# Kernel tuning notes

Hardware: AMD Instinct MI355X
Metric: run time of the kernel (lower is better)

## Reference

```python
import jax, jax.numpy as jnp
import numpy as np

N_EXPERTS = 8
D_MODEL = 1024
D_FF = 2048
NUM_TOKENS = 16384


def setup_inputs() -> dict:
    key = jax.random.key(0)
    k1, k2, k3, k4 = jax.random.split(key, 4)
    x = jax.random.normal(k1, (NUM_TOKENS, D_MODEL), dtype=jnp.float32)
    expert_indices = jax.random.randint(k2, (NUM_TOKENS,), 0, N_EXPERTS, dtype=jnp.int32)
    # init per nn.init.normal_(std=0.02)
    gate_up_weight = 0.02 * jax.random.normal(k3, (N_EXPERTS, 2 * D_FF, D_MODEL), dtype=jnp.float32)
    down_weight = 0.02 * jax.random.normal(k4, (N_EXPERTS, D_MODEL, D_FF), dtype=jnp.float32)
    return {"x": x, "expert_indices": expert_indices,
            "gate_up_weight": gate_up_weight, "down_weight": down_weight}


def reference(x, expert_indices, gate_up_weight, down_weight):
    # Faithful math: each token t uses expert e = expert_indices[t]:
    #   combined = x @ gate_up_weight[e].T ; gate, up = split ; h = silu(gate)*up
    #   out = h @ down_weight[e].T
    # Implemented as a fixed loop over the (small) expert set with masked
    # accumulation, avoiding the original's per-token [2F,D] weight gather.
    n_experts = gate_up_weight.shape[0]
    d_ff = down_weight.shape[2]
    out = jnp.zeros((x.shape[0], down_weight.shape[1]), dtype=x.dtype)
    for e in range(n_experts):
        combined = x @ gate_up_weight[e].T                  # [T, 2*d_ff]
        gate, up = combined[:, :d_ff], combined[:, d_ff:]
        hidden = jax.nn.silu(gate) * up                     # [T, d_ff]
        o = hidden @ down_weight[e].T                       # [T, d_model]
        out = out + jnp.where((expert_indices == e)[:, None], o, 0.0)
    return out
```

## Files before the change

### kernel.cpp

```cpp
#include <hip/hip_runtime.h>

#define NTOK 16384
#define DM 1024
#define DFF 2048
#define NE 8

typedef unsigned short u16;
typedef __attribute__((ext_vector_type(8))) short bf16x8;
typedef __attribute__((ext_vector_type(4))) float f32x4;

__device__ __forceinline__ u16 f2bf(float f) {
  unsigned u = __float_as_uint(f);
  u += 0x7fff + ((u >> 16) & 1);
  return (u16)(u >> 16);
}

__device__ __forceinline__ void async16(const void* g, void* l) {
  __builtin_amdgcn_global_load_lds(
      (const __attribute__((address_space(1))) unsigned int*)g,
      (__attribute__((address_space(3))) unsigned int*)l, 16, 0, 0);
}

__global__ void k_count(const int* __restrict__ idx, int* __restrict__ counts) {
  int t = blockIdx.x * 256 + threadIdx.x;
  atomicAdd(&counts[idx[t]], 1);
}

__global__ void k_offsets(int* __restrict__ c) {
  if (threadIdx.x == 0) {
    int acc = 0;
    for (int e = 0; e < NE; e++) { c[8 + e] = acc; c[16 + e] = acc; acc += c[e]; }
  }
}

__global__ void k_scatter(const int* __restrict__ idx, int* __restrict__ cursor,
                          int* __restrict__ tl) {
  int t = blockIdx.x * 256 + threadIdx.x;
  int pos = atomicAdd(&cursor[idx[t]], 1);
  tl[pos] = t;
}

__global__ void k_cvt(const float* __restrict__ s, u16* __restrict__ d) {
  size_t i = ((size_t)blockIdx.x * 256 + threadIdx.x) * 4;
  float4 v = *(const float4*)(s + i);
  ushort4 o;
  o.x = f2bf(v.x); o.y = f2bf(v.y); o.z = f2bf(v.z); o.w = f2bf(v.w);
  *(ushort4*)(d + i) = o;
}

__global__ __launch_bounds__(512, 2) void k_gemm1(
    const u16* __restrict__ xb, const u16* __restrict__ wgu,
    u16* __restrict__ hid, const int* __restrict__ tl,
    const int* __restrict__ offs, const int* __restrict__ counts) {
  int wg = blockIdx.x;
  int e = wg & 7;
  int r = wg >> 3;
  int by = r / 9;
  int bx = r - by * 9;
  int Me = counts[e];
  int m0 = bx * 256;
  if (m0 >= Me) return;
  int n0 = by * 128;
  int oe = offs[e];
  const int* tle = tl + oe;

  int tid = threadIdx.x;
  int lane = tid & 63;
  int wid = tid >> 6;
  int wm = wid >> 2;
  int wn = wid & 3;

  __shared__ u16 lds[2][2][256 * 64];

  int lr = lane >> 3;
  int swz = ((lane & 7) ^ lr) * 8;
  const u16* pA[4];
  const u16* pB[4];
#pragma unroll
  for (int j = 0; j < 4; j++) {
    int c = j * 8 + wid;
    int a = m0 + c * 8 + lr;
    if (a >= Me) a = Me - 1;
    pA[j] = xb + (size_t)tle[a] * DM + swz;
    int b = c * 8 + lr;
    int grow = ((b >> 5) & 1) * DFF + n0 + ((b >> 6) & 3) * 32 + (b & 31);
    pB[j] = wgu + ((size_t)e * 2 * DFF + grow) * DM + swz;
  }

  f32x4 acc[8][4];
#pragma unroll
  for (int m = 0; m < 8; m++)
#pragma unroll
    for (int f = 0; f < 4; f++) acc[m][f] = (f32x4){0.f, 0.f, 0.f, 0.f};

  const int r15 = lane & 15;
  const int hi4 = lane >> 4;
  const int rx = r15 & 7;

#pragma unroll
  for (int j = 0; j < 4; j++) {
    int off = (j * 8 + wid) * 1024;
    async16(pA[j], (char*)&lds[0][0][0] + off);
    async16(pB[j], (char*)&lds[0][1][0] + off);
  }
  asm volatile("s_waitcnt vmcnt(0)" ::: "memory");
  __builtin_amdgcn_s_barrier();
  __builtin_amdgcn_sched_barrier(0);

  int cur = 0;
#pragma unroll 1
  for (int t = 0; t < DM / 64; t++) {
    const char* Ab = (const char*)&lds[cur][0][0];
    const char* Bb = (const char*)&lds[cur][1][0];
    char* LA = (char*)&lds[cur ^ 1][0][0];
    char* LB = (char*)&lds[cur ^ 1][1][0];
    int k1 = (t + 1) * 64;
    bool pf = (t < DM / 64 - 1);
    bf16x8 bfr[4][2];
#pragma unroll
    for (int p = 0; p < 4; p++) {
      if (p == 0) {
#pragma unroll
        for (int f = 0; f < 4; f++)
#pragma unroll
          for (int kk = 0; kk < 2; kk++) {
            int row = wn * 64 + f * 16 + r15;
            bfr[f][kk] = *(const bf16x8*)(Bb + row * 128 + (((kk * 4 + hi4) ^ rx) * 16));
          }
      }
      bf16x8 af[2][2];
#pragma unroll
      for (int i = 0; i < 2; i++)
#pragma unroll
        for (int kk = 0; kk < 2; kk++) {
          int row = wm * 128 + (2 * p + i) * 16 + r15;
          af[i][kk] = *(const bf16x8*)(Ab + row * 128 + (((kk * 4 + hi4) ^ rx) * 16));
        }
      if (pf && p < 2) {
#pragma unroll
        for (int j = 0; j < 2; j++) {
          int jj = p * 2 + j;
          int off = (jj * 8 + wid) * 1024;
          async16(pA[jj] + k1, LA + off);
          async16(pB[jj] + k1, LB + off);
        }
      }
      __builtin_amdgcn_s_barrier();
      __builtin_amdgcn_sched_barrier(0);
      __builtin_amdgcn_s_setprio(1);
#pragma unroll
      for (int kk = 0; kk < 2; kk++)
#pragma unroll
        for (int i = 0; i < 2; i++)
#pragma unroll
          for (int f = 0; f < 4; f++)
            acc[2 * p + i][f] = __builtin_amdgcn_mfma_f32_16x16x32_bf16(
                af[i][kk], bfr[f][kk], acc[2 * p + i][f], 0, 0, 0);
      __builtin_amdgcn_s_setprio(0);
      __builtin_amdgcn_sched_barrier(0);
      if (p < 3) {
        __builtin_amdgcn_s_barrier();
        __builtin_amdgcn_sched_barrier(0);
      }
    }
    asm volatile("s_waitcnt vmcnt(0)" ::: "memory");
    __builtin_amdgcn_s_barrier();
    __builtin_amdgcn_sched_barrier(0);
    cur ^= 1;
  }

  int colb = n0 + wn * 32 + r15;
#pragma unroll
  for (int m = 0; m < 8; m++) {
#pragma unroll
    for (int rr = 0; rr < 4; rr++) {
      int gm = m0 + wm * 128 + m * 16 + hi4 * 4 + rr;
      if (gm < Me) {
        size_t rowp = (size_t)(oe + gm) * DFF;
#pragma unroll
        for (int f = 0; f < 2; f++) {
          float g = acc[m][f][rr];
          float u = acc[m][f + 2][rr];
          float s = g / (1.0f + __expf(-g));
          hid[rowp + colb + f * 16] = f2bf(s * u);
        }
      }
    }
  }
}

__global__ __launch_bounds__(512, 2) void k_gemm2(
    const u16* __restrict__ hid, const u16* __restrict__ wd,
    float* __restrict__ out, const int* __restrict__ tl,
    const int* __restrict__ offs, const int* __restrict__ counts) {
  int wg = blockIdx.x;
  int e = wg & 7;
  int r = wg >> 3;
  int by = r / 9;
  int bx = r - by * 9;
  int Me = counts[e];
  int m0 = bx * 256;
  if (m0 >= Me) return;
  int n0 = by * 128;
  int oe = offs[e];
  const int* tle = tl + oe;

  int tid = threadIdx.x;
  int lane = tid & 63;
  int wid = tid >> 6;
  int wm = wid >> 1;
  int wn = wid & 1;

  __shared__ u16 ldsA[2][256 * 64];
  __shared__ u16 ldsB[2][128 * 64];

  int lr = lane >> 3;
  int swz = ((lane & 7) ^ lr) * 8;
  const u16* pA[4];
  const u16* pB[2];
#pragma unroll
  for (int j = 0; j < 4; j++) {
    int c = j * 8 + wid;
    int a = m0 + c * 8 + lr;
    if (a >= Me) a = Me - 1;
    pA[j] = hid + (size_t)(oe + a) * DFF + swz;
  }
#pragma unroll
  for (int j = 0; j < 2; j++) {
    int c = j * 8 + wid;
    pB[j] = wd + ((size_t)e * DM + n0 + c * 8 + lr) * DFF + swz;
  }

  f32x4 acc[4][4];
#pragma unroll
  for (int m = 0; m < 4; m++)
#pragma unroll
    for (int f = 0; f < 4; f++) acc[m][f] = (f32x4){0.f, 0.f, 0.f, 0.f};

  const int r15 = lane & 15;
  const int hi4 = lane >> 4;
  const int rx = r15 & 7;

#pragma unroll
  for (int j = 0; j < 4; j++)
    async16(pA[j], (char*)&ldsA[0][0] + (j * 8 + wid) * 1024);
#pragma unroll
  for (int j = 0; j < 2; j++)
    async16(pB[j], (char*)&ldsB[0][0] + (j * 8 + wid) * 1024);
  asm volatile("s_waitcnt vmcnt(0)" ::: "memory");
  __builtin_amdgcn_s_barrier();
  __builtin_amdgcn_sched_barrier(0);

  int cur = 0;
#pragma unroll 1
  for (int t = 0; t < DFF / 64; t++) {
    const char* Ab = (const char*)&ldsA[cur][0];
    const char* Bb = (const char*)&ldsB[cur][0];
    char* LA = (char*)&ldsA[cur ^ 1][0];
    char* LB = (char*)&ldsB[cur ^ 1][0];
    int k1 = (t + 1) * 64;
    bool pf = (t < DFF / 64 - 1);
    bf16x8 bfr[4][2];
#pragma unroll
    for (int p = 0; p < 2; p++) {
      if (p == 0) {
#pragma unroll
        for (int f = 0; f < 4; f++)
#pragma unroll
          for (int kk = 0; kk < 2; kk++) {
            int row = wn * 64 + f * 16 + r15;
            bfr[f][kk] = *(const bf16x8*)(Bb + row * 128 + (((kk * 4 + hi4) ^ rx) * 16));
          }
      }
      bf16x8 af[2][2];
#pragma unroll
      for (int i = 0; i < 2; i++)
#pragma unroll
        for (int kk = 0; kk < 2; kk++) {
          int row = wm * 64 + (2 * p + i) * 16 + r15;
          af[i][kk] = *(const bf16x8*)(Ab + row * 128 + (((kk * 4 + hi4) ^ rx) * 16));
        }
      if (pf) {
#pragma unroll
        for (int j = 0; j < 2; j++) {
          int jj = p * 2 + j;
          async16(pA[jj] + k1, LA + (jj * 8 + wid) * 1024);
        }
        async16(pB[p] + k1, LB + (p * 8 + wid) * 1024);
      }
      __builtin_amdgcn_s_barrier();
      __builtin_amdgcn_sched_barrier(0);
      __builtin_amdgcn_s_setprio(1);
#pragma unroll
      for (int kk = 0; kk < 2; kk++)
#pragma unroll
        for (int i = 0; i < 2; i++)
#pragma unroll
          for (int f = 0; f < 4; f++)
            acc[2 * p + i][f] = __builtin_amdgcn_mfma_f32_16x16x32_bf16(
                af[i][kk], bfr[f][kk], acc[2 * p + i][f], 0, 0, 0);
      __builtin_amdgcn_s_setprio(0);
      __builtin_amdgcn_sched_barrier(0);
      if (p < 1) {
        __builtin_amdgcn_s_barrier();
        __builtin_amdgcn_sched_barrier(0);
      }
    }
    asm volatile("s_waitcnt vmcnt(0)" ::: "memory");
    __builtin_amdgcn_s_barrier();
    __builtin_amdgcn_sched_barrier(0);
    cur ^= 1;
  }

  int colb = n0 + wn * 64 + r15;
#pragma unroll
  for (int m = 0; m < 4; m++) {
#pragma unroll
    for (int rr = 0; rr < 4; rr++) {
      int gm = m0 + wm * 64 + m * 16 + hi4 * 4 + rr;
      if (gm < Me) {
        int tk = tle[gm];
#pragma unroll
        for (int f = 0; f < 4; f++)
          out[(size_t)tk * DM + colb + f * 16] = acc[m][f][rr];
      }
    }
  }
}

extern "C" void kernel_launch(void* const* d_in, const int* in_sizes, int n_in,
                              void* d_out, int out_size, void* d_ws, size_t ws_size,
                              hipStream_t stream) {
  const float* x   = (const float*)d_in[0];
  const int* eidx  = (const int*)d_in[1];
  const float* wgu = (const float*)d_in[2];
  const float* wd  = (const float*)d_in[3];
  float* out = (float*)d_out;
  char* ws = (char*)d_ws;

  int* ctrl = (int*)ws;
  int* toklist = (int*)(ws + 256);
  u16* xb   = (u16*)(ws + 65792);
  u16* wgub = (u16*)(ws + 65792 + 33554432ull);
  u16* wdb  = (u16*)(ws + 65792 + 33554432ull + 67108864ull);
  u16* hid  = (u16*)(ws + 65792 + 33554432ull + 67108864ull + 33554432ull);

  hipMemsetAsync(ws, 0, 256, stream);
  k_count<<<NTOK / 256, 256, 0, stream>>>(eidx, ctrl);
  k_offsets<<<1, 64, 0, stream>>>(ctrl);
  k_scatter<<<NTOK / 256, 256, 0, stream>>>(eidx, ctrl + 16, toklist);

  k_cvt<<<(NTOK * DM) / 1024, 256, 0, stream>>>(x, xb);
  k_cvt<<<(NE * 2 * DFF * DM) / 1024, 256, 0, stream>>>(wgu, wgub);
  k_cvt<<<(NE * DM * DFF) / 1024, 256, 0, stream>>>(wd, wdb);

  k_gemm1<<<9 * 16 * NE, 512, 0, stream>>>(xb, wgub, hid, toklist, ctrl + 8, ctrl);
  k_gemm2<<<9 * 8 * NE, 512, 0, stream>>>(hid, wdb, out, toklist, ctrl + 8, ctrl);
}
```

Baseline: 503.7 us.

## Enlarge gemm2 tiles, drop mid-iteration barriers, fuse conversion kernels, reorder grid

The three fp32-to-bf16 conversion kernels are merged into one grid-stride kernel, saving two launches. gemm2 moves from a 256x128 to a 256x256 output tile with 8 accumulator rows per wave, halving its block count and the number of times the hidden activations are re-read. In both GEMMs the prefetch is spread evenly across all phases and the barriers between phases are removed. The block-index decode also changes so that adjacent blocks walk the N dimension within the same M tile. The cost is more register pressure in gemm2 and fewer blocks to fill the GPU, and dropping the intra-loop barriers may introduce LDS hazards.

```diff
diff --git a/kernel.cpp b/kernel.cpp
--- a/kernel.cpp
+++ b/kernel.cpp
@@ -40,12 +40,26 @@
   tl[pos] = t;
 }
 
-__global__ void k_cvt(const float* __restrict__ s, u16* __restrict__ d) {
-  size_t i = ((size_t)blockIdx.x * 256 + threadIdx.x) * 4;
-  float4 v = *(const float4*)(s + i);
-  ushort4 o;
-  o.x = f2bf(v.x); o.y = f2bf(v.y); o.z = f2bf(v.z); o.w = f2bf(v.w);
-  *(ushort4*)(d + i) = o;
+__global__ void k_cvt_all(const float* __restrict__ x, const float* __restrict__ wgu,
+                          const float* __restrict__ wd, u16* __restrict__ xb,
+                          u16* __restrict__ wgub, u16* __restrict__ wdb) {
+  const size_t N1 = (size_t)NTOK * DM;
+  const size_t N2 = (size_t)NE * 2 * DFF * DM;
+  const size_t N3 = (size_t)NE * DM * DFF;
+  const size_t total4 = (N1 + N2 + N3) / 4;
+  for (size_t q = (size_t)blockIdx.x * 256 + threadIdx.x; q < total4;
+       q += (size_t)gridDim.x * 256) {
+    size_t i = q * 4;
+    const float* s;
+    u16* d;
+    if (i < N1) { s = x + i; d = xb + i; }
+    else if (i < N1 + N2) { s = wgu + (i - N1); d = wgub + (i - N1); }
+    else { s = wd + (i - N1 - N2); d = wdb + (i - N1 - N2); }
+    float4 v = *(const float4*)s;
+    ushort4 o;
+    o.x = f2bf(v.x); o.y = f2bf(v.y); o.z = f2bf(v.z); o.w = f2bf(v.w);
+    *(ushort4*)d = o;
+  }
 }
 
 __global__ __launch_bounds__(512, 2) void k_gemm1(
@@ -55,8 +69,8 @@
   int wg = blockIdx.x;
   int e = wg & 7;
   int r = wg >> 3;
-  int by = r / 9;
-  int bx = r - by * 9;
+  int bx = r >> 4;
+  int by = r & 15;
   int Me = counts[e];
   int m0 = bx * 256;
   if (m0 >= Me) return;
@@ -136,14 +150,10 @@
           int row = wm * 128 + (2 * p + i) * 16 + r15;
           af[i][kk] = *(const bf16x8*)(Ab + row * 128 + (((kk * 4 + hi4) ^ rx) * 16));
         }
-      if (pf && p < 2) {
-#pragma unroll
-        for (int j = 0; j < 2; j++) {
-          int jj = p * 2 + j;
-          int off = (jj * 8 + wid) * 1024;
-          async16(pA[jj] + k1, LA + off);
-          async16(pB[jj] + k1, LB + off);
-        }
+      if (pf) {
+        int off = (p * 8 + wid) * 1024;
+        async16(pA[p] + k1, LA + off);
+        async16(pB[p] + k1, LB + off);
       }
       __builtin_amdgcn_s_barrier();
       __builtin_amdgcn_sched_barrier(0);
@@ -158,10 +168,6 @@
                 af[i][kk], bfr[f][kk], acc[2 * p + i][f], 0, 0, 0);
       __builtin_amdgcn_s_setprio(0);
       __builtin_amdgcn_sched_barrier(0);
-      if (p < 3) {
-        __builtin_amdgcn_s_barrier();
-        __builtin_amdgcn_sched_barrier(0);
-      }
     }
     asm volatile("s_waitcnt vmcnt(0)" ::: "memory");
     __builtin_amdgcn_s_barrier();
@@ -196,44 +202,39 @@
   int wg = blockIdx.x;
   int e = wg & 7;
   int r = wg >> 3;
-  int by = r / 9;
-  int bx = r - by * 9;
+  int bx = r >> 2;
+  int by = r & 3;
   int Me = counts[e];
   int m0 = bx * 256;
   if (m0 >= Me) return;
-  int n0 = by * 128;
+  int n0 = by * 256;
   int oe = offs[e];
   const int* tle = tl + oe;
 
   int tid = threadIdx.x;
   int lane = tid & 63;
   int wid = tid >> 6;
-  int wm = wid >> 1;
-  int wn = wid & 1;
-
-  __shared__ u16 ldsA[2][256 * 64];
-  __shared__ u16 ldsB[2][128 * 64];
+  int wm = wid >> 2;
+  int wn = wid & 3;
+
+  __shared__ u16 lds[2][2][256 * 64];
 
   int lr = lane >> 3;
   int swz = ((lane & 7) ^ lr) * 8;
   const u16* pA[4];
-  const u16* pB[2];
+  const u16* pB[4];
 #pragma unroll
   for (int j = 0; j < 4; j++) {
     int c = j * 8 + wid;
     int a = m0 + c * 8 + lr;
     if (a >= Me) a = Me - 1;
     pA[j] = hid + (size_t)(oe + a) * DFF + swz;
-  }
-#pragma unroll
-  for (int j = 0; j < 2; j++) {
-    int c = j * 8 + wid;
     pB[j] = wd + ((size_t)e * DM + n0 + c * 8 + lr) * DFF + swz;
   }
 
-  f32x4 acc[4][4];
-#pragma unroll
-  for (int m = 0; m < 4; m++)
+  f32x4 acc[8][4];
+#pragma unroll
+  for (int m = 0; m < 8; m++)
 #pragma unroll
     for (int f = 0; f < 4; f++) acc[m][f] = (f32x4){0.f, 0.f, 0.f, 0.f};
 
@@ -242,11 +243,11 @@
   const int rx = r15 & 7;
 
 #pragma unroll
-  for (int j = 0; j < 4; j++)
-    async16(pA[j], (char*)&ldsA[0][0] + (j * 8 + wid) * 1024);
-#pragma unroll
-  for (int j = 0; j < 2; j++)
-    async16(pB[j], (char*)&ldsB[0][0] + (j * 8 + wid) * 1024);
+  for (int j = 0; j < 4; j++) {
+    int off = (j * 8 + wid) * 1024;
+    async16(pA[j], (char*)&lds[0][0][0] + off);
+    async16(pB[j], (char*)&lds[0][1][0] + off);
+  }
   asm volatile("s_waitcnt vmcnt(0)" ::: "memory");
   __builtin_amdgcn_s_barrier();
   __builtin_amdgcn_sched_barrier(0);
@@ -254,15 +255,15 @@
   int cur = 0;
 #pragma unroll 1
   for (int t = 0; t < DFF / 64; t++) {
-    const char* Ab = (const char*)&ldsA[cur][0];
-    const char* Bb = (const char*)&ldsB[cur][0];
-    char* LA = (char*)&ldsA[cur ^ 1][0];
-    char* LB = (char*)&ldsB[cur ^ 1][0];
+    const char* Ab = (const char*)&lds[cur][0][0];
+    const char* Bb = (const char*)&lds[cur][1][0];
+    char* LA = (char*)&lds[cur ^ 1][0][0];
+    char* LB = (char*)&lds[cur ^ 1][1][0];
     int k1 = (t + 1) * 64;
     bool pf = (t < DFF / 64 - 1);
     bf16x8 bfr[4][2];
 #pragma unroll
-    for (int p = 0; p < 2; p++) {
+    for (int p = 0; p < 4; p++) {
       if (p == 0) {
 #pragma unroll
         for (int f = 0; f < 4; f++)
@@ -277,16 +278,13 @@
       for (int i = 0; i < 2; i++)
 #pragma unroll
         for (int kk = 0; kk < 2; kk++) {
-          int row = wm * 64 + (2 * p + i) * 16 + r15;
+          int row = wm * 128 + (2 * p + i) * 16 + r15;
           af[i][kk] = *(const bf16x8*)(Ab + row * 128 + (((kk * 4 + hi4) ^ rx) * 16));
         }
       if (pf) {
-#pragma unroll
-        for (int j = 0; j < 2; j++) {
-          int jj = p * 2 + j;
-          async16(pA[jj] + k1, LA + (jj * 8 + wid) * 1024);
-        }
-        async16(pB[p] + k1, LB + (p * 8 + wid) * 1024);
+        int off = (p * 8 + wid) * 1024;
+        async16(pA[p] + k1, LA + off);
+        async16(pB[p] + k1, LB + off);
       }
       __builtin_amdgcn_s_barrier();
       __builtin_amdgcn_sched_barrier(0);
@@ -301,10 +299,6 @@
                 af[i][kk], bfr[f][kk], acc[2 * p + i][f], 0, 0, 0);
       __builtin_amdgcn_s_setprio(0);
       __builtin_amdgcn_sched_barrier(0);
-      if (p < 1) {
-        __builtin_amdgcn_s_barrier();
-        __builtin_amdgcn_sched_barrier(0);
-      }
     }
     asm volatile("s_waitcnt vmcnt(0)" ::: "memory");
     __builtin_amdgcn_s_barrier();
@@ -314,10 +308,10 @@
 
   int colb = n0 + wn * 64 + r15;
 #pragma unroll
-  for (int m = 0; m < 4; m++) {
+  for (int m = 0; m < 8; m++) {
 #pragma unroll
     for (int rr = 0; rr < 4; rr++) {
-      int gm = m0 + wm * 64 + m * 16 + hi4 * 4 + rr;
+      int gm = m0 + wm * 128 + m * 16 + hi4 * 4 + rr;
       if (gm < Me) {
         int tk = tle[gm];
 #pragma unroll
@@ -350,10 +344,8 @@
   k_offsets<<<1, 64, 0, stream>>>(ctrl);
   k_scatter<<<NTOK / 256, 256, 0, stream>>>(eidx, ctrl + 16, toklist);
 
-  k_cvt<<<(NTOK * DM) / 1024, 256, 0, stream>>>(x, xb);
-  k_cvt<<<(NE * 2 * DFF * DM) / 1024, 256, 0, stream>>>(wgu, wgub);
-  k_cvt<<<(NE * DM * DFF) / 1024, 256, 0, stream>>>(wd, wdb);
+  k_cvt_all<<<2048, 256, 0, stream>>>(x, wgu, wd, xb, wgub, wdb);
 
   k_gemm1<<<9 * 16 * NE, 512, 0, stream>>>(xb, wgub, hid, toklist, ctrl + 8, ctrl);
-  k_gemm2<<<9 * 8 * NE, 512, 0, stream>>>(hid, wdb, out, toklist, ctrl + 8, ctrl);
-}
+  k_gemm2<<<9 * 4 * NE, 512, 0, stream>>>(hid, wdb, out, toklist, ctrl + 8, ctrl);
+}
```

Result: no change. 499.7 us (-0.8%).
